# Kernel tuning notes

Measured on AMD Instinct MI355X. Metric: run time of the kernel, lower is better.

Reference implementation:

```python
import jax, jax.numpy as jnp
import numpy as np

N = 50000      # current-level nodes
N_NEXT = 2000  # next-level nodes
E = 1600000    # directed edges (before self-loops)
D_IN = 128
D_OUT = 128
LN_EPS = 1e-5


def setup_inputs() -> dict:
    key = jax.random.key(0)
    ks = jax.random.split(key, 12)
    curr_h = jax.random.normal(ks[0], (N, D_IN), dtype=jnp.float32)
    next_h = jax.random.normal(ks[1], (N_NEXT, D_IN), dtype=jnp.float32)
    inc = jax.random.uniform(ks[2], (N, N_NEXT), dtype=jnp.float32)
    src = jax.random.randint(ks[3], (E,), 0, N, dtype=jnp.int64)
    dst = jax.random.randint(ks[4], (E,), 0, N, dtype=jnp.int64)
    s = 1.0 / np.sqrt(D_IN)
    W_conv = jax.random.normal(ks[5], (D_IN, D_OUT), dtype=jnp.float32) * s
    b_conv = jnp.zeros((D_OUT,), dtype=jnp.float32)
    W_fus = jax.random.normal(ks[6], (D_IN, D_OUT), dtype=jnp.float32) * s
    b_fus = jnp.zeros((D_OUT,), dtype=jnp.float32)
    conv_w = jax.random.uniform(ks[7], (D_OUT,), dtype=jnp.float32)
    topDown_w = jax.random.uniform(ks[8], (D_OUT,), dtype=jnp.float32)
    ln_gamma = jnp.ones((D_OUT,), dtype=jnp.float32)
    ln_beta = jnp.zeros((D_OUT,), dtype=jnp.float32)
    return {
        "curr_h": curr_h, "next_h": next_h, "inc": inc,
        "src": src, "dst": dst,
        "W_conv": W_conv, "b_conv": b_conv,
        "W_fus": W_fus, "b_fus": b_fus,
        "conv_w": conv_w, "topDown_w": topDown_w,
        "ln_gamma": ln_gamma, "ln_beta": ln_beta,
    }


def _graph_conv(x, W, b, src_sl, dst_sl, norm_out, norm_in):
    # DGL GraphConv, norm='both': D_out^{-1/2} on src, sum-aggregate, D_in^{-1/2} on dst.
    h = x @ W                               # [N, D_OUT]
    h = h * norm_out[:, None]
    agg = jax.ops.segment_sum(h[src_sl], dst_sl, num_segments=N)  # SpMM
    return agg * norm_in[:, None] + b


def reference(curr_h, next_h, inc, src, dst,
              W_conv, b_conv, W_fus, b_fus,
              conv_w, topDown_w, ln_gamma, ln_beta):
    # dgl.add_self_loop
    loop = jnp.arange(N, dtype=src.dtype)
    src_sl = jnp.concatenate([src, loop])
    dst_sl = jnp.concatenate([dst, loop])
    ones = jnp.ones_like(src_sl, dtype=jnp.float32)
    out_deg = jax.ops.segment_sum(ones, src_sl, num_segments=N)
    in_deg = jax.ops.segment_sum(ones, dst_sl, num_segments=N)
    norm_out = jax.lax.rsqrt(out_deg)  # >=1 due to self-loops
    norm_in = jax.lax.rsqrt(in_deg)

    conv_layer = _graph_conv(curr_h, W_conv, b_conv, src_sl, dst_sl, norm_out, norm_in) * conv_w[None, :]
    fused_in = inc @ next_h  # dense incidence matmul [N, D_IN]
    top_down = _graph_conv(fused_in, W_fus, b_fus, src_sl, dst_sl, norm_out, norm_in) * topDown_w[None, :]

    result = conv_layer + top_down
    # LayerNorm over last dim
    mu = jnp.mean(result, axis=-1, keepdims=True)
    var = jnp.mean((result - mu) ** 2, axis=-1, keepdims=True)
    result = (result - mu) * jax.lax.rsqrt(var + LN_EPS) * ln_gamma + ln_beta
    # dropout p=0.0 (eval) -> identity; activation ReLU
    return jax.nn.relu(result)
```

## Files before the change

### kernel.cpp

```cpp
#include <hip/hip_runtime.h>
#include <hip/hip_bf16.h>

#define N_NODES   50000
#define EDGES     1600000
#define D         128
#define K_INC     2000
#define K_TOT     2128
#define K_PAD     2176
#define KTILES    34
#define LN_EPS    1e-5f

typedef float f32x4 __attribute__((ext_vector_type(4)));
typedef short short8 __attribute__((ext_vector_type(8)));
typedef ushort ushort8v __attribute__((ext_vector_type(8)));

__device__ __forceinline__ ushort f2bf(float x) {
    return __hip_bfloat16_raw(__float2bfloat16(x)).x;
}
__device__ __forceinline__ float bf_lo(uint v) { return __uint_as_float(v << 16); }
__device__ __forceinline__ float bf_hi(uint v) { return __uint_as_float(v & 0xffff0000u); }

#define GLOAD_LDS16(gp, lp) \
    __builtin_amdgcn_global_load_lds((const __attribute__((address_space(1))) void*)(gp), \
                                     (__attribute__((address_space(3))) void*)(lp), 16, 0, 0)

__global__ void probe_kernel(const int* __restrict__ src, int* __restrict__ flag) {
    __shared__ int any_nonzero;
    if (threadIdx.x == 0) any_nonzero = 0;
    __syncthreads();
    int v = src[threadIdx.x * 2 + 1];
    if (v != 0) any_nonzero = 1;
    __syncthreads();
    if (threadIdx.x == 0) flag[0] = any_nonzero ? 0 : 1;
}

__global__ void zero_kernel(int* __restrict__ p, int n) {
    int i = blockIdx.x * 256 + threadIdx.x;
    if (i < n) p[i] = 0;
}

__global__ void deg_kernel(const int* __restrict__ src, const int* __restrict__ dst,
                           const int* __restrict__ flag,
                           int* __restrict__ out_deg, int* __restrict__ in_cnt) {
    int e = blockIdx.x * 256 + threadIdx.x;
    int st = 1 + flag[0];
    if (e < EDGES) {
        atomicAdd(&out_deg[src[e * st]], 1);
        atomicAdd(&in_cnt[dst[e * st]], 1);
    }
}

__global__ __launch_bounds__(1024) void scan_kernel(const int* __restrict__ cnt,
                                                    int* __restrict__ row_start) {
    __shared__ int buf[1024];
    int t = threadIdx.x;
    const int N = N_NODES;
    int chunk = (N + 1023) / 1024;
    int lo = t * chunk, hi = min(lo + chunk, N);
    int s = 0;
    for (int i = lo; i < hi; ++i) s += cnt[i];
    buf[t] = s;
    __syncthreads();
    for (int off = 1; off < 1024; off <<= 1) {
        int v = (t >= off) ? buf[t - off] : 0;
        __syncthreads();
        buf[t] += v;
        __syncthreads();
    }
    int run = (t > 0) ? buf[t - 1] : 0;
    for (int i = lo; i < hi; ++i) { row_start[i] = run; run += cnt[i]; }
    if (t == 1023) row_start[N] = buf[1023];
}

__global__ void fill_kernel(const int* __restrict__ src, const int* __restrict__ dst,
                            const int* __restrict__ flag,
                            const int* __restrict__ row_start, int* __restrict__ cursor,
                            int* __restrict__ csr_src) {
    int e = blockIdx.x * 256 + threadIdx.x;
    int st = 1 + flag[0];
    if (e < EDGES) {
        int d = dst[e * st];
        int pos = atomicAdd(&cursor[d], 1);
        csr_src[row_start[d] + pos] = src[e * st];
    }
}

#define PKB 16
__global__ __launch_bounds__(128) void p_kernel(
    const float* __restrict__ next_h, const float* __restrict__ W_fus,
    const float* __restrict__ topDown_w, const float* __restrict__ W_conv,
    const float* __restrict__ conv_w, ushort* __restrict__ PbT) {
    int n = threadIdx.x;
    int k0 = blockIdx.x * PKB;
    if (k0 < K_INC) {
        float acc[PKB];
#pragma unroll
        for (int t = 0; t < PKB; ++t) acc[t] = 0.f;
        for (int j = 0; j < D; ++j) {
            float w = W_fus[(size_t)j * D + n];
#pragma unroll
            for (int t = 0; t < PKB; ++t)
                acc[t] += next_h[(size_t)(k0 + t) * D + j] * w;
        }
        float tw = topDown_w[n];
#pragma unroll
        for (int t = 0; t < PKB; ++t)
            PbT[(size_t)n * K_PAD + k0 + t] = f2bf(acc[t] * tw);
    } else if (k0 < K_TOT) {
        float cw = conv_w[n];
#pragma unroll
        for (int t = 0; t < PKB; ++t)
            PbT[(size_t)n * K_PAD + k0 + t] = f2bf(W_conv[(size_t)(k0 + t - K_INC) * D + n] * cw);
    } else {
#pragma unroll
        for (int t = 0; t < PKB; ++t)
            PbT[(size_t)n * K_PAD + k0 + t] = 0;
    }
}

__global__ __launch_bounds__(256, 3) void gemm_kernel(
    const float* __restrict__ inc, const float* __restrict__ curr_h,
    const ushort* __restrict__ PbT, const int* __restrict__ out_deg,
    ushort* __restrict__ Zs) {
    __shared__ __align__(16) ushort As[2][64][72];
    __shared__ __align__(16) ushort Bs[2][128 * 64];
    const int N = N_NODES;
    int tid = threadIdx.x;
    int wave = tid >> 6, lane = tid & 63;
    int wm = wave >> 1, wn = wave & 1;
    int r = lane & 15, q = lane >> 4;
    int rowBase = blockIdx.x * 64;

    f32x4 acc[2][4] = {};
    float4 aReg[2][2];

    auto stage_issue = [&](int kt, int nb) {
        int k0 = kt * 64;
#pragma unroll
        for (int it = 0; it < 2; ++it) {
            int u = tid + it * 256;
            int arow = u >> 3, c8 = u & 7;
            int gk = k0 + c8 * 8;
            int grow = rowBase + arow; if (grow >= N) grow = N - 1;
            if (gk < K_INC) {
                const float4* p4 = (const float4*)(inc + (size_t)grow * K_INC + gk);
                aReg[it][0] = p4[0]; aReg[it][1] = p4[1];
            } else if (gk < K_TOT) {
                const float4* p4 = (const float4*)(curr_h + (size_t)grow * D + (gk - K_INC));
                aReg[it][0] = p4[0]; aReg[it][1] = p4[1];
            } else {
                aReg[it][0] = make_float4(0.f, 0.f, 0.f, 0.f);
                aReg[it][1] = make_float4(0.f, 0.f, 0.f, 0.f);
            }
        }
#pragma unroll
        for (int it = 0; it < 4; ++it) {
            int chunk = tid + it * 256;
            int n = chunk >> 3;
            int c16 = (chunk & 7) << 4;
            int gb = c16 ^ ((n & 7) << 4);
            const char* gp = (const char*)PbT + (size_t)n * (K_PAD * 2) + (size_t)(k0 * 2) + gb;
            char* lp = (char*)(&Bs[nb][0]) + it * 4096 + wave * 1024;
            GLOAD_LDS16(gp, lp);
        }
    };
    auto stage_write = [&](int nb) {
#pragma unroll
        for (int it = 0; it < 2; ++it) {
            int u = tid + it * 256;
            int arow = u >> 3, c8 = u & 7;
            const float* f = (const float*)&aReg[it][0];
            ushort8v hv;
#pragma unroll
            for (int j = 0; j < 8; ++j) hv[j] = f2bf(f[j]);
            *(ushort8v*)&As[nb][arow][c8 * 8] = hv;
        }
    };

    stage_issue(0, 0);
    stage_write(0);
    __syncthreads();

    int cur = 0;
    for (int kt = 0; kt < KTILES; ++kt) {
        int nb = cur ^ 1;
        if (kt + 1 < KTILES) stage_issue(kt + 1, nb);
#pragma unroll
        for (int kk = 0; kk < 2; ++kk) {
            short8 af[2], bfr[4];
#pragma unroll
            for (int mi = 0; mi < 2; ++mi)
                af[mi] = *(const short8*)&As[cur][wm * 32 + mi * 16 + r][kk * 32 + q * 8];
#pragma unroll
            for (int ni = 0; ni < 4; ++ni) {
                int brow = wn * 64 + ni * 16 + r;
                int bcol = (kk * 64 + q * 16) ^ ((r & 7) << 4);
                bfr[ni] = *(const short8*)((const char*)&Bs[cur][0] + brow * 128 + bcol);
            }
#pragma unroll
            for (int mi = 0; mi < 2; ++mi)
#pragma unroll
                for (int ni = 0; ni < 4; ++ni)
                    acc[mi][ni] = __builtin_amdgcn_mfma_f32_16x16x32_bf16(af[mi], bfr[ni], acc[mi][ni], 0, 0, 0);
        }
        if (kt + 1 < KTILES) stage_write(nb);
        __syncthreads();
        cur = nb;
    }

#pragma unroll
    for (int mi = 0; mi < 2; ++mi) {
#pragma unroll
        for (int j = 0; j < 4; ++j) {
            int grow = rowBase + wm * 32 + mi * 16 + q * 4 + j;
            if (grow < N) {
                float no = rsqrtf((float)(out_deg[grow] + 1));
#pragma unroll
                for (int ni = 0; ni < 4; ++ni) {
                    int col = wn * 64 + ni * 16 + r;
                    Zs[(size_t)grow * D + col] = f2bf(acc[mi][ni][j] * no);
                }
            }
        }
    }
}

__global__ __launch_bounds__(256) void agg_ln_kernel(
    const ushort* __restrict__ Zs, const int* __restrict__ row_start,
    const int* __restrict__ csr_src,
    const float* __restrict__ b_conv, const float* __restrict__ b_fus,
    const float* __restrict__ conv_w, const float* __restrict__ topDown_w,
    const float* __restrict__ gamma, const float* __restrict__ beta,
    float* __restrict__ out) {
    int wid = threadIdx.x >> 6, lane = threadIdx.x & 63;
    int node = blockIdx.x * 4 + wid;
    if (node >= N_NODES) return;
    int c0 = lane * 2;

    uint v = *(const uint*)(Zs + (size_t)node * D + c0);
    float a0 = bf_lo(v), a1 = bf_hi(v);
    int beg = row_start[node], end = row_start[node + 1];

    for (int base = beg; base < end; base += 64) {
        int rem = end - base;
        int cnt = rem < 64 ? rem : 64;
        int idx = 0;
        if (base + lane < end) idx = csr_src[base + lane];
        int i = 0;
        for (; i + 4 <= cnt; i += 4) {
            int s0 = __shfl(idx, i),     s1 = __shfl(idx, i + 1);
            int s2 = __shfl(idx, i + 2), s3 = __shfl(idx, i + 3);
            uint v0 = *(const uint*)(Zs + (size_t)s0 * D + c0);
            uint v1 = *(const uint*)(Zs + (size_t)s1 * D + c0);
            uint v2 = *(const uint*)(Zs + (size_t)s2 * D + c0);
            uint v3 = *(const uint*)(Zs + (size_t)s3 * D + c0);
            a0 += bf_lo(v0) + bf_lo(v1) + bf_lo(v2) + bf_lo(v3);
            a1 += bf_hi(v0) + bf_hi(v1) + bf_hi(v2) + bf_hi(v3);
        }
        for (; i < cnt; ++i) {
            int s0 = __shfl(idx, i);
            uint v0 = *(const uint*)(Zs + (size_t)s0 * D + c0);
            a0 += bf_lo(v0); a1 += bf_hi(v0);
        }
    }

    float nin = rsqrtf((float)(end - beg + 1));
    float y0 = a0 * nin + b_conv[c0] * conv_w[c0] + b_fus[c0] * topDown_w[c0];
    float y1 = a1 * nin + b_conv[c0 + 1] * conv_w[c0 + 1] + b_fus[c0 + 1] * topDown_w[c0 + 1];

    float s1v = y0 + y1, s2v = y0 * y0 + y1 * y1;
#pragma unroll
    for (int off = 1; off < 64; off <<= 1) {
        s1v += __shfl_xor(s1v, off);
        s2v += __shfl_xor(s2v, off);
    }
    float mu = s1v * (1.f / D);
    float var = s2v * (1.f / D) - mu * mu;
    float rstd = rsqrtf(var + LN_EPS);
    float r0 = (y0 - mu) * rstd * gamma[c0] + beta[c0];
    float r1 = (y1 - mu) * rstd * gamma[c0 + 1] + beta[c0 + 1];
    *(float2*)(out + (size_t)node * D + c0) = make_float2(fmaxf(r0, 0.f), fmaxf(r1, 0.f));
}

extern "C" void kernel_launch(void* const* d_in, const int* in_sizes, int n_in,
                              void* d_out, int out_size, void* d_ws, size_t ws_size,
                              hipStream_t stream) {
    const float* curr_h    = (const float*)d_in[0];
    const float* next_h    = (const float*)d_in[1];
    const float* inc       = (const float*)d_in[2];
    const int*   src       = (const int*)d_in[3];
    const int*   dst       = (const int*)d_in[4];
    const float* W_conv    = (const float*)d_in[5];
    const float* b_conv    = (const float*)d_in[6];
    const float* W_fus     = (const float*)d_in[7];
    const float* b_fus     = (const float*)d_in[8];
    const float* conv_w    = (const float*)d_in[9];
    const float* topDown_w = (const float*)d_in[10];
    const float* ln_gamma  = (const float*)d_in[11];
    const float* ln_beta   = (const float*)d_in[12];

    const int N = N_NODES;
    const int E = EDGES;

    char* p = (char*)d_ws;
    ushort* Zs = (ushort*)p;     p += (size_t)N * D * sizeof(ushort);
    ushort* PbT = (ushort*)p;    p += (size_t)D * K_PAD * 2;
    int* out_deg   = (int*)p;    p += (size_t)N * 4;
    int* in_cnt    = (int*)p;    p += (size_t)N * 4;
    int* cursor    = (int*)p;    p += (size_t)N * 4;
    int* row_start = (int*)p;    p += (size_t)(N + 1) * 4;
    int* idx_flag  = (int*)p;    p += 256;
    int* csr_src   = (int*)p;    p += (size_t)E * 4;

    probe_kernel<<<1, 1024, 0, stream>>>(src, idx_flag);
    zero_kernel<<<(3 * N + 255) / 256, 256, 0, stream>>>(out_deg, 3 * N);
    deg_kernel<<<(E + 255) / 256, 256, 0, stream>>>(src, dst, idx_flag, out_deg, in_cnt);
    scan_kernel<<<1, 1024, 0, stream>>>(in_cnt, row_start);
    fill_kernel<<<(E + 255) / 256, 256, 0, stream>>>(src, dst, idx_flag, row_start, cursor, csr_src);
    p_kernel<<<K_PAD / PKB, 128, 0, stream>>>(next_h, W_fus, topDown_w, W_conv, conv_w, PbT);
    gemm_kernel<<<(N + 63) / 64, 256, 0, stream>>>(inc, curr_h, PbT, out_deg, Zs);
    agg_ln_kernel<<<(N + 3) / 4, 256, 0, stream>>>(Zs, row_start, csr_src,
                                                   b_conv, b_fus, conv_w, topDown_w,
                                                   ln_gamma, ln_beta, (float*)d_out);
}
```

Before: 954.0 us.

## Vectorize aggregation with 16-lane groups per node and move out-degree counting into fill

The aggregation kernel now assigns 16 lanes to each node, four nodes per wavefront, and each lane loads 16-byte vectors of 8 bf16 features instead of 4-byte pairs. This cuts the number of gather instructions and makes more row loads independent. The degree and fill kernels each handle two edges per thread with vector index loads. Out-degree atomics move from the degree pass into the fill pass, so the degree pass only reads dst. The cost is lane divergence inside a wavefront when the four nodes have different degrees, since the loop runs to the largest one. There is also no bounds check on node, which happens to be safe because N is a multiple of 16.

```diff
diff --git a/kernel.cpp b/kernel.cpp
--- a/kernel.cpp
+++ b/kernel.cpp
@@ -39,15 +39,21 @@
     if (i < n) p[i] = 0;
 }
 
-__global__ void deg_kernel(const int* __restrict__ src, const int* __restrict__ dst,
-                           const int* __restrict__ flag,
-                           int* __restrict__ out_deg, int* __restrict__ in_cnt) {
-    int e = blockIdx.x * 256 + threadIdx.x;
-    int st = 1 + flag[0];
-    if (e < EDGES) {
-        atomicAdd(&out_deg[src[e * st]], 1);
-        atomicAdd(&in_cnt[dst[e * st]], 1);
-    }
+__global__ void deg_kernel(const int* __restrict__ dst, const int* __restrict__ flag,
+                           int* __restrict__ in_cnt) {
+    int t = blockIdx.x * 256 + threadIdx.x;
+    int e0 = t * 2;
+    if (e0 >= EDGES) return;
+    int d0, d1;
+    if (flag[0]) {
+        int4 v = *(const int4*)(dst + (size_t)e0 * 2);
+        d0 = v.x; d1 = v.z;
+    } else {
+        int2 v = *(const int2*)(dst + e0);
+        d0 = v.x; d1 = v.y;
+    }
+    atomicAdd(&in_cnt[d0], 1);
+    atomicAdd(&in_cnt[d1], 1);
 }
 
 __global__ __launch_bounds__(1024) void scan_kernel(const int* __restrict__ cnt,
@@ -75,14 +81,26 @@
 __global__ void fill_kernel(const int* __restrict__ src, const int* __restrict__ dst,
                             const int* __restrict__ flag,
                             const int* __restrict__ row_start, int* __restrict__ cursor,
-                            int* __restrict__ csr_src) {
-    int e = blockIdx.x * 256 + threadIdx.x;
-    int st = 1 + flag[0];
-    if (e < EDGES) {
-        int d = dst[e * st];
-        int pos = atomicAdd(&cursor[d], 1);
-        csr_src[row_start[d] + pos] = src[e * st];
-    }
+                            int* __restrict__ out_deg, int* __restrict__ csr_src) {
+    int t = blockIdx.x * 256 + threadIdx.x;
+    int e0 = t * 2;
+    if (e0 >= EDGES) return;
+    int s0, s1, d0, d1;
+    if (flag[0]) {
+        int4 vs = *(const int4*)(src + (size_t)e0 * 2);
+        int4 vd = *(const int4*)(dst + (size_t)e0 * 2);
+        s0 = vs.x; s1 = vs.z; d0 = vd.x; d1 = vd.z;
+    } else {
+        int2 vs = *(const int2*)(src + e0);
+        int2 vd = *(const int2*)(dst + e0);
+        s0 = vs.x; s1 = vs.y; d0 = vd.x; d1 = vd.y;
+    }
+    atomicAdd(&out_deg[s0], 1);
+    int p0 = atomicAdd(&cursor[d0], 1);
+    csr_src[row_start[d0] + p0] = s0;
+    atomicAdd(&out_deg[s1], 1);
+    int p1 = atomicAdd(&cursor[d1], 1);
+    csr_src[row_start[d1] + p1] = s1;
 }
 
 #define PKB 16
@@ -232,54 +250,105 @@
     const float* __restrict__ conv_w, const float* __restrict__ topDown_w,
     const float* __restrict__ gamma, const float* __restrict__ beta,
     float* __restrict__ out) {
-    int wid = threadIdx.x >> 6, lane = threadIdx.x & 63;
-    int node = blockIdx.x * 4 + wid;
-    if (node >= N_NODES) return;
-    int c0 = lane * 2;
-
-    uint v = *(const uint*)(Zs + (size_t)node * D + c0);
-    float a0 = bf_lo(v), a1 = bf_hi(v);
+    int tid = threadIdx.x;
+    int wid = tid >> 6, lane = tid & 63;
+    int sl = lane & 15;
+    int g = lane >> 4;
+    int node = blockIdx.x * 16 + wid * 4 + g;
+    int c0 = sl * 8;
+
+    float a[8];
+    {
+        uint4 v = *(const uint4*)(Zs + (size_t)node * D + c0);
+        a[0] = bf_lo(v.x); a[1] = bf_hi(v.x);
+        a[2] = bf_lo(v.y); a[3] = bf_hi(v.y);
+        a[4] = bf_lo(v.z); a[5] = bf_hi(v.z);
+        a[6] = bf_lo(v.w); a[7] = bf_hi(v.w);
+    }
+
     int beg = row_start[node], end = row_start[node + 1];
-
-    for (int base = beg; base < end; base += 64) {
-        int rem = end - base;
-        int cnt = rem < 64 ? rem : 64;
+    int deg = end - beg;
+    int m = max(deg, __shfl_xor(deg, 16));
+    m = max(m, __shfl_xor(m, 32));
+    int srcbase = lane & 48;
+
+    for (int base = 0; base < m; base += 16) {
         int idx = 0;
-        if (base + lane < end) idx = csr_src[base + lane];
-        int i = 0;
-        for (; i + 4 <= cnt; i += 4) {
-            int s0 = __shfl(idx, i),     s1 = __shfl(idx, i + 1);
-            int s2 = __shfl(idx, i + 2), s3 = __shfl(idx, i + 3);
-            uint v0 = *(const uint*)(Zs + (size_t)s0 * D + c0);
-            uint v1 = *(const uint*)(Zs + (size_t)s1 * D + c0);
-            uint v2 = *(const uint*)(Zs + (size_t)s2 * D + c0);
-            uint v3 = *(const uint*)(Zs + (size_t)s3 * D + c0);
-            a0 += bf_lo(v0) + bf_lo(v1) + bf_lo(v2) + bf_lo(v3);
-            a1 += bf_hi(v0) + bf_hi(v1) + bf_hi(v2) + bf_hi(v3);
-        }
-        for (; i < cnt; ++i) {
-            int s0 = __shfl(idx, i);
-            uint v0 = *(const uint*)(Zs + (size_t)s0 * D + c0);
-            a0 += bf_lo(v0); a1 += bf_hi(v0);
-        }
-    }
-
-    float nin = rsqrtf((float)(end - beg + 1));
-    float y0 = a0 * nin + b_conv[c0] * conv_w[c0] + b_fus[c0] * topDown_w[c0];
-    float y1 = a1 * nin + b_conv[c0 + 1] * conv_w[c0 + 1] + b_fus[c0 + 1] * topDown_w[c0 + 1];
-
-    float s1v = y0 + y1, s2v = y0 * y0 + y1 * y1;
-#pragma unroll
-    for (int off = 1; off < 64; off <<= 1) {
+        if (base + sl < deg) idx = csr_src[beg + base + sl];
+        int cnt = deg - base;
+        if (cnt >= 16) {
+#pragma unroll
+            for (int i = 0; i < 16; i += 4) {
+                int s0 = __shfl(idx, srcbase + i);
+                int s1 = __shfl(idx, srcbase + i + 1);
+                int s2 = __shfl(idx, srcbase + i + 2);
+                int s3 = __shfl(idx, srcbase + i + 3);
+                uint4 v0 = *(const uint4*)(Zs + (size_t)s0 * D + c0);
+                uint4 v1 = *(const uint4*)(Zs + (size_t)s1 * D + c0);
+                uint4 v2 = *(const uint4*)(Zs + (size_t)s2 * D + c0);
+                uint4 v3 = *(const uint4*)(Zs + (size_t)s3 * D + c0);
+                a[0] += bf_lo(v0.x) + bf_lo(v1.x) + bf_lo(v2.x) + bf_lo(v3.x);
+                a[1] += bf_hi(v0.x) + bf_hi(v1.x) + bf_hi(v2.x) + bf_hi(v3.x);
+                a[2] += bf_lo(v0.y) + bf_lo(v1.y) + bf_lo(v2.y) + bf_lo(v3.y);
+                a[3] += bf_hi(v0.y) + bf_hi(v1.y) + bf_hi(v2.y) + bf_hi(v3.y);
+                a[4] += bf_lo(v0.z) + bf_lo(v1.z) + bf_lo(v2.z) + bf_lo(v3.z);
+                a[5] += bf_hi(v0.z) + bf_hi(v1.z) + bf_hi(v2.z) + bf_hi(v3.z);
+                a[6] += bf_lo(v0.w) + bf_lo(v1.w) + bf_lo(v2.w) + bf_lo(v3.w);
+                a[7] += bf_hi(v0.w) + bf_hi(v1.w) + bf_hi(v2.w) + bf_hi(v3.w);
+            }
+        } else if (cnt > 0) {
+            for (int i = 0; i < cnt; ++i) {
+                int s0 = __shfl(idx, srcbase + i);
+                uint4 v0 = *(const uint4*)(Zs + (size_t)s0 * D + c0);
+                a[0] += bf_lo(v0.x); a[1] += bf_hi(v0.x);
+                a[2] += bf_lo(v0.y); a[3] += bf_hi(v0.y);
+                a[4] += bf_lo(v0.z); a[5] += bf_hi(v0.z);
+                a[6] += bf_lo(v0.w); a[7] += bf_hi(v0.w);
+            }
+        }
+    }
+
+    float nin = rsqrtf((float)(deg + 1));
+    float4 bc0 = *(const float4*)(b_conv + c0),   bc1 = *(const float4*)(b_conv + c0 + 4);
+    float4 cw0 = *(const float4*)(conv_w + c0),   cw1 = *(const float4*)(conv_w + c0 + 4);
+    float4 bf0 = *(const float4*)(b_fus + c0),    bf1 = *(const float4*)(b_fus + c0 + 4);
+    float4 tw0 = *(const float4*)(topDown_w + c0),tw1 = *(const float4*)(topDown_w + c0 + 4);
+    float bias[8] = {
+        bc0.x * cw0.x + bf0.x * tw0.x, bc0.y * cw0.y + bf0.y * tw0.y,
+        bc0.z * cw0.z + bf0.z * tw0.z, bc0.w * cw0.w + bf0.w * tw0.w,
+        bc1.x * cw1.x + bf1.x * tw1.x, bc1.y * cw1.y + bf1.y * tw1.y,
+        bc1.z * cw1.z + bf1.z * tw1.z, bc1.w * cw1.w + bf1.w * tw1.w };
+    float y[8];
+    float s1v = 0.f, s2v = 0.f;
+#pragma unroll
+    for (int j = 0; j < 8; ++j) {
+        y[j] = a[j] * nin + bias[j];
+        s1v += y[j]; s2v += y[j] * y[j];
+    }
+#pragma unroll
+    for (int off = 1; off < 16; off <<= 1) {
         s1v += __shfl_xor(s1v, off);
         s2v += __shfl_xor(s2v, off);
     }
     float mu = s1v * (1.f / D);
     float var = s2v * (1.f / D) - mu * mu;
     float rstd = rsqrtf(var + LN_EPS);
-    float r0 = (y0 - mu) * rstd * gamma[c0] + beta[c0];
-    float r1 = (y1 - mu) * rstd * gamma[c0 + 1] + beta[c0 + 1];
-    *(float2*)(out + (size_t)node * D + c0) = make_float2(fmaxf(r0, 0.f), fmaxf(r1, 0.f));
+    float4 ga0 = *(const float4*)(gamma + c0), ga1 = *(const float4*)(gamma + c0 + 4);
+    float4 be0 = *(const float4*)(beta + c0),  be1 = *(const float4*)(beta + c0 + 4);
+    float gam[8] = { ga0.x, ga0.y, ga0.z, ga0.w, ga1.x, ga1.y, ga1.z, ga1.w };
+    float bet[8] = { be0.x, be0.y, be0.z, be0.w, be1.x, be1.y, be1.z, be1.w };
+    float4 o0, o1;
+    float r;
+    r = (y[0] - mu) * rstd * gam[0] + bet[0]; o0.x = fmaxf(r, 0.f);
+    r = (y[1] - mu) * rstd * gam[1] + bet[1]; o0.y = fmaxf(r, 0.f);
+    r = (y[2] - mu) * rstd * gam[2] + bet[2]; o0.z = fmaxf(r, 0.f);
+    r = (y[3] - mu) * rstd * gam[3] + bet[3]; o0.w = fmaxf(r, 0.f);
+    r = (y[4] - mu) * rstd * gam[4] + bet[4]; o1.x = fmaxf(r, 0.f);
+    r = (y[5] - mu) * rstd * gam[5] + bet[5]; o1.y = fmaxf(r, 0.f);
+    r = (y[6] - mu) * rstd * gam[6] + bet[6]; o1.z = fmaxf(r, 0.f);
+    r = (y[7] - mu) * rstd * gam[7] + bet[7]; o1.w = fmaxf(r, 0.f);
+    *(float4*)(out + (size_t)node * D + c0) = o0;
+    *(float4*)(out + (size_t)node * D + c0 + 4) = o1;
 }
 
 extern "C" void kernel_launch(void* const* d_in, const int* in_sizes, int n_in,
@@ -314,12 +383,13 @@
 
     probe_kernel<<<1, 1024, 0, stream>>>(src, idx_flag);
     zero_kernel<<<(3 * N + 255) / 256, 256, 0, stream>>>(out_deg, 3 * N);
-    deg_kernel<<<(E + 255) / 256, 256, 0, stream>>>(src, dst, idx_flag, out_deg, in_cnt);
+    deg_kernel<<<(E / 2 + 255) / 256, 256, 0, stream>>>(dst, idx_flag, in_cnt);
     scan_kernel<<<1, 1024, 0, stream>>>(in_cnt, row_start);
-    fill_kernel<<<(E + 255) / 256, 256, 0, stream>>>(src, dst, idx_flag, row_start, cursor, csr_src);
+    fill_kernel<<<(E / 2 + 255) / 256, 256, 0, stream>>>(src, dst, idx_flag, row_start,
+                                                         cursor, out_deg, csr_src);
     p_kernel<<<K_PAD / PKB, 128, 0, stream>>>(next_h, W_fus, topDown_w, W_conv, conv_w, PbT);
     gemm_kernel<<<(N + 63) / 64, 256, 0, stream>>>(inc, curr_h, PbT, out_deg, Zs);
-    agg_ln_kernel<<<(N + 3) / 4, 256, 0, stream>>>(Zs, row_start, csr_src,
-                                                   b_conv, b_fus, conv_w, topDown_w,
-                                                   ln_gamma, ln_beta, (float*)d_out);
-}
+    agg_ln_kernel<<<(N + 15) / 16, 256, 0, stream>>>(Zs, row_start, csr_src,
+                                                     b_conv, b_fus, conv_w, topDown_w,
+                                                     ln_gamma, ln_beta, (float*)d_out);
+}
```

Result: slower. 978.5 us (+2.6%).
